# Kernel tuning notes

Measured on AMD Instinct MI355X. Metric: run time of the kernel, lower is better.

Reference implementation:

```python
import jax, jax.numpy as jnp
import numpy as np

N_PAPER = 100000
N_AUTHOR = 50000
E = 800000
D_IN, D_HID, D_OUT = 128, 128, 64


def seg_max(x, src, dst, num_segments):
    # adj_t.matmul(x, reduce='max'): per-destination max over neighbor features;
    # destinations with no in-edges get 0 (torch_sparse convention).
    m = jax.ops.segment_max(x[src], dst, num_segments=num_segments)
    return jnp.where(jnp.isneginf(m), jnp.zeros((), m.dtype), m)


def setup_inputs() -> dict:
    key = jax.random.key(0)
    ks = jax.random.split(key, 32)
    inp = {}
    inp['x_paper'] = jax.random.normal(ks[0], (N_PAPER, D_IN), jnp.float32)
    inp['emb_author'] = jax.random.normal(ks[1], (N_AUTHOR, D_IN), jnp.float32)
    inp['writes_src'] = jax.random.randint(ks[2], (E,), 0, N_AUTHOR, jnp.int32)
    inp['writes_dst'] = jax.random.randint(ks[3], (E,), 0, N_PAPER, jnp.int32)
    inp['cites_src'] = jax.random.randint(ks[4], (E,), 0, N_PAPER, jnp.int32)
    inp['cites_dst'] = jax.random.randint(ks[5], (E,), 0, N_PAPER, jnp.int32)
    inp['wb_src'] = jax.random.randint(ks[6], (E,), 0, N_PAPER, jnp.int32)
    inp['wb_dst'] = jax.random.randint(ks[7], (E,), 0, N_AUTHOR, jnp.int32)

    def lin_w(k, din, dout):
        s = 1.0 / np.sqrt(din)
        return jax.random.uniform(k, (din, dout), jnp.float32, -s, s)

    # layer 1: D_IN -> D_HID
    inp['w1_rel_writes'] = lin_w(ks[8], D_IN, D_HID)
    inp['w1_rel_cites'] = lin_w(ks[9], D_IN, D_HID)
    inp['w1_rel_wb'] = lin_w(ks[10], D_IN, D_HID)
    inp['w1_root_paper'] = lin_w(ks[11], D_IN, D_HID)
    inp['b1_root_paper'] = jnp.zeros((D_HID,), jnp.float32)
    inp['w1_root_author'] = lin_w(ks[12], D_IN, D_HID)
    inp['b1_root_author'] = jnp.zeros((D_HID,), jnp.float32)
    # layer 2: D_HID -> D_OUT
    inp['w2_rel_writes'] = lin_w(ks[13], D_HID, D_OUT)
    inp['w2_rel_cites'] = lin_w(ks[14], D_HID, D_OUT)
    inp['w2_rel_wb'] = lin_w(ks[15], D_HID, D_OUT)
    inp['w2_root_paper'] = lin_w(ks[16], D_HID, D_OUT)
    inp['b2_root_paper'] = jnp.zeros((D_OUT,), jnp.float32)
    inp['w2_root_author'] = lin_w(ks[17], D_HID, D_OUT)
    inp['b2_root_author'] = jnp.zeros((D_OUT,), jnp.float32)
    return inp


def _conv(xp, xa, edges, w_writes, w_cites, w_wb, w_rp, b_rp, w_ra, b_ra):
    writes_src, writes_dst, cites_src, cites_dst, wb_src, wb_dst = edges
    out_p = xp @ w_rp + b_rp
    out_a = xa @ w_ra + b_ra
    out_p = out_p + seg_max(xa, writes_src, writes_dst, N_PAPER) @ w_writes
    out_p = out_p + seg_max(xp, cites_src, cites_dst, N_PAPER) @ w_cites
    out_a = out_a + seg_max(xp, wb_src, wb_dst, N_AUTHOR) @ w_wb
    return out_p, out_a


def reference(x_paper, emb_author,
              writes_src, writes_dst, cites_src, cites_dst, wb_src, wb_dst,
              w1_rel_writes, w1_rel_cites, w1_rel_wb,
              w1_root_paper, b1_root_paper, w1_root_author, b1_root_author,
              w2_rel_writes, w2_rel_cites, w2_rel_wb,
              w2_root_paper, b2_root_paper, w2_root_author, b2_root_author):
    edges = (writes_src, writes_dst, cites_src, cites_dst, wb_src, wb_dst)
    hp, ha = _conv(x_paper, emb_author, edges,
                   w1_rel_writes, w1_rel_cites, w1_rel_wb,
                   w1_root_paper, b1_root_paper, w1_root_author, b1_root_author)
    hp, ha = jax.nn.relu(hp), jax.nn.relu(ha)  # dropout p=0 -> identity
    return _conv(hp, ha, edges,
                 w2_rel_writes, w2_rel_cites, w2_rel_wb,
                 w2_root_paper, b2_root_paper, w2_root_author, b2_root_author)
```

## Files before the change

### kernel.cpp

```cpp
#include <hip/hip_runtime.h>


#define DI 128
#define NP 100000
#define NA 50000
#define EPB 4096
#define MAXBIN 391

typedef short s8v __attribute__((ext_vector_type(8)));
typedef float f32x4 __attribute__((ext_vector_type(4)));

__device__ __forceinline__ unsigned short bf16_rne(float f) {
  unsigned int fb = __float_as_uint(f);
  fb += 0x7FFFu + ((fb >> 16) & 1u);
  return (unsigned short)(fb >> 16);
}

__global__ __launch_bounds__(256) void cvt2_k(const float* __restrict__ Xp,
                                              unsigned short* __restrict__ Yp, int n4p,
                                              const float* __restrict__ Xa,
                                              unsigned short* __restrict__ Ya, int n4a) {
  int i = blockIdx.x * 256 + threadIdx.x;
  const float* X; unsigned short* Y;
  if (i < n4p) { X = Xp; Y = Yp; }
  else { i -= n4p; if (i >= n4a) return; X = Xa; Y = Ya; }
  float4 f = reinterpret_cast<const float4*>(X)[i];
  ushort4 o;
  o.x = bf16_rne(f.x); o.y = bf16_rne(f.y); o.z = bf16_rne(f.z); o.w = bf16_rne(f.w);
  reinterpret_cast<ushort4*>(Y)[i] = o;
}

struct R3Args {
  const int* src[3]; const int* dst[3];
  int* bh[3]; int* bhs[3];
  unsigned int* tmp[3];
  int* bkt[3]; int* cnt[3]; int* rs[3];
  int E[3]; int N[3]; int nbin[3]; int NB[3];
};

__global__ __launch_bounds__(256) void radix_s1_k(R3Args a) {
  int y = blockIdx.y, blk = blockIdx.x;
  int NB = a.NB[y];
  if (blk >= NB) return;
  __shared__ int hist[MAXBIN];
  int nbin = a.nbin[y];
  for (int i = threadIdx.x; i < nbin; i += 256) hist[i] = 0;
  __syncthreads();
  int e0 = blk * EPB, e1 = min(e0 + EPB, a.E[y]);
  const int* dst = a.dst[y];
  for (int e = e0 + threadIdx.x; e < e1; e += 256)
    atomicAdd(&hist[dst[e] >> 8], 1);
  __syncthreads();
  int* bh = a.bh[y];
  for (int i = threadIdx.x; i < nbin; i += 256) bh[i * NB + blk] = hist[i];
}

__global__ __launch_bounds__(256) void radix_x1_k(R3Args a) {
  int y = blockIdx.y, blk = blockIdx.x;
  int NB = a.NB[y];
  if (blk >= NB) return;
  __shared__ int cur[MAXBIN];
  int nbin = a.nbin[y];
  const int* bhs = a.bhs[y];
  for (int i = threadIdx.x; i < nbin; i += 256) cur[i] = bhs[i * NB + blk];
  __syncthreads();
  int e0 = blk * EPB, e1 = min(e0 + EPB, a.E[y]);
  const int* dst = a.dst[y];
  const int* src = a.src[y];
  unsigned int* tmp = a.tmp[y];
  for (int e = e0 + threadIdx.x; e < e1; e += 256) {
    int d = dst[e];
    int pos = atomicAdd(&cur[d >> 8], 1);
    tmp[pos] = ((unsigned int)(d & 255) << 24) | (unsigned int)src[e];
  }
}

__global__ __launch_bounds__(256) void radix_p2_k(R3Args a) {
  int y = blockIdx.y, bin = blockIdx.x;
  if (bin >= a.nbin[y]) return;
  __shared__ int hist[256], scn[256], cursor[256];
  int t = threadIdx.x;
  hist[t] = 0;
  __syncthreads();
  const int* bhs = a.bhs[y];
  int NB = a.NB[y];
  int base = bhs[bin * NB];
  int end  = (bin + 1 < a.nbin[y]) ? bhs[(bin + 1) * NB] : a.E[y];
  const unsigned int* tmp = a.tmp[y];
  for (int i = base + t; i < end; i += 256)
    atomicAdd(&hist[tmp[i] >> 24], 1);
  __syncthreads();
  int v = hist[t];
  scn[t] = v; __syncthreads();
  int acc = v;
  for (int o = 1; o < 256; o <<= 1) {
    int u = (t >= o) ? scn[t - o] : 0;
    __syncthreads();
    acc += u; scn[t] = acc;
    __syncthreads();
  }
  int ex = acc - v;
  cursor[t] = ex;
  int d = bin * 256 + t;
  if (d < a.N[y]) { a.cnt[y][d] = v; a.rs[y][d] = base + ex; }
  __syncthreads();
  int* bkt = a.bkt[y];
  for (int i = base + t; i < end; i += 256) {
    unsigned int p = tmp[i];
    int pos = atomicAdd(&cursor[p >> 24], 1);
    bkt[base + pos] = (int)(p & 0xFFFFFFu);
  }
}

struct S3Args {
  const int* cnt[3]; int* bsum[3]; int* rs[3];
  int n[3]; int nb[3];
};

__global__ __launch_bounds__(256) void blocksum3_k(S3Args a) {
  int y = blockIdx.y;
  int n = a.n[y];
  if (blockIdx.x * 1024 >= n) return;
  __shared__ int red[256];
  int t = threadIdx.x;
  int base = blockIdx.x * 1024 + t * 4;
  int s = 0;
  #pragma unroll
  for (int i = 0; i < 4; ++i) { int idx = base + i; if (idx < n) s += a.cnt[y][idx]; }
  red[t] = s; __syncthreads();
  #pragma unroll
  for (int o = 128; o > 0; o >>= 1) { if (t < o) red[t] += red[t + o]; __syncthreads(); }
  if (t == 0) a.bsum[y][blockIdx.x] = red[0];
}

__global__ __launch_bounds__(256) void partials3_k(S3Args a) {
  __shared__ int sm[256];
  int y = blockIdx.x;
  int nb = a.nb[y];
  int t = threadIdx.x;
  int v = (t < nb) ? a.bsum[y][t] : 0;
  sm[t] = v; __syncthreads();
  int acc = v;
  for (int o = 1; o < 256; o <<= 1) {
    int u = (t >= o) ? sm[t - o] : 0;
    __syncthreads();
    acc += u; sm[t] = acc;
    __syncthreads();
  }
  if (t < nb) a.bsum[y][t] = acc - v;
}

__global__ __launch_bounds__(256) void scanwrite3_k(S3Args a) {
  int y = blockIdx.y;
  int n = a.n[y];
  if (blockIdx.x * 1024 >= n) return;
  __shared__ int ts[256];
  int t = threadIdx.x;
  int base = blockIdx.x * 1024 + t * 4;
  int v[4]; int s = 0;
  #pragma unroll
  for (int i = 0; i < 4; ++i) { int idx = base + i; v[i] = (idx < n) ? a.cnt[y][idx] : 0; s += v[i]; }
  ts[t] = s; __syncthreads();
  int inc = s;
  for (int o = 1; o < 256; o <<= 1) {
    int u = (t >= o) ? ts[t - o] : 0;
    __syncthreads();
    inc += u; ts[t] = inc;
    __syncthreads();
  }
  int p = a.bsum[y][blockIdx.x] + inc - s;
  #pragma unroll
  for (int i = 0; i < 4; ++i) { int idx = base + i; if (idx < n) { a.rs[y][idx] = p; p += v[i]; } }
}

struct G3Args {
  const int* cnt[3]; const int* rs[3]; const int* bkt[3];
  const unsigned short* X[3]; unsigned short* S[3];
  int N[3];
};

__global__ __launch_bounds__(256) void gather3_k(G3Args a) {
  const int y = blockIdx.y;
  const int lane = threadIdx.x & 63;
  const int wave = threadIdx.x >> 6;
  const int g = lane >> 4, lg = lane & 15;
  const int d = blockIdx.x * 16 + wave * 4 + g;
  if (d >= a.N[y]) return;

  unsigned short* So = a.S[y] + (size_t)d * DI + lg * 8;
  const int deg = a.cnt[y][d];
  if (deg == 0) {
    uint4 z; z.x = z.y = z.z = z.w = 0u;
    *reinterpret_cast<uint4*>(So) = z;
    return;
  }
  const int* bp = a.bkt[y] + a.rs[y][d];
  const unsigned short* X = a.X[y];

  float ml[4], mh[4];
  #pragma unroll
  for (int j = 0; j < 4; ++j) { ml[j] = -3.4e38f; mh[j] = -3.4e38f; }

  int s0 = bp[0];
  for (int e = 0; e < deg; e += 4) {
    int s1 = (e + 1 < deg) ? bp[e + 1] : s0;
    int s2 = (e + 2 < deg) ? bp[e + 2] : s0;
    int s3 = (e + 3 < deg) ? bp[e + 3] : s0;
    int sn = (e + 4 < deg) ? bp[e + 4] : s0;
    uint4 r0 = *reinterpret_cast<const uint4*>(X + (size_t)s0 * DI + lg * 8);
    uint4 r1 = *reinterpret_cast<const uint4*>(X + (size_t)s1 * DI + lg * 8);
    uint4 r2 = *reinterpret_cast<const uint4*>(X + (size_t)s2 * DI + lg * 8);
    uint4 r3 = *reinterpret_cast<const uint4*>(X + (size_t)s3 * DI + lg * 8);
    unsigned int w0[4] = {r0.x, r0.y, r0.z, r0.w};
    unsigned int w1[4] = {r1.x, r1.y, r1.z, r1.w};
    unsigned int w2[4] = {r2.x, r2.y, r2.z, r2.w};
    unsigned int w3[4] = {r3.x, r3.y, r3.z, r3.w};
    #pragma unroll
    for (int j = 0; j < 4; ++j) {
      float a0 = fmaxf(__uint_as_float(w0[j] << 16), __uint_as_float(w1[j] << 16));
      float a1 = fmaxf(__uint_as_float(w2[j] << 16), __uint_as_float(w3[j] << 16));
      ml[j] = fmaxf(ml[j], fmaxf(a0, a1));
      float b0 = fmaxf(__uint_as_float(w0[j] & 0xFFFF0000u), __uint_as_float(w1[j] & 0xFFFF0000u));
      float b1 = fmaxf(__uint_as_float(w2[j] & 0xFFFF0000u), __uint_as_float(w3[j] & 0xFFFF0000u));
      mh[j] = fmaxf(mh[j], fmaxf(b0, b1));
    }
    s0 = sn;
  }
  uint4 o;
  o.x = (__float_as_uint(ml[0]) >> 16) | (__float_as_uint(mh[0]) & 0xFFFF0000u);
  o.y = (__float_as_uint(ml[1]) >> 16) | (__float_as_uint(mh[1]) & 0xFFFF0000u);
  o.z = (__float_as_uint(ml[2]) >> 16) | (__float_as_uint(mh[2]) & 0xFFFF0000u);
  o.w = (__float_as_uint(ml[3]) >> 16) | (__float_as_uint(mh[3]) & 0xFFFF0000u);
  *reinterpret_cast<uint4*>(So) = o;
}

struct WArgs {
  const float* w[10];
  unsigned short* wf[10];
};
__global__ __launch_bounds__(256) void warrange_k(WArgs args) {
  int widx = blockIdx.y;
  int OUTi = (widx < 5) ? 128 : 64;
  int CF = OUTi / 16;
  int nt = 4 * CF * 64;
  int t = blockIdx.x * 256 + threadIdx.x;
  if (t >= nt) return;
  int lane = t & 63, tmp = t >> 6;
  int cf = tmp % CF, kc = tmp / CF;
  int k0 = kc * 32 + (lane >> 4) * 8;
  int c  = cf * 16 + (lane & 15);
  const float* w = args.w[widx];
  s8v v;
  #pragma unroll
  for (int i = 0; i < 8; ++i) v[i] = (short)bf16_rne(w[(k0 + i) * OUTi + c]);
  *(reinterpret_cast<s8v*>(args.wf[widx]) + t) = v;
}

template<int CF>
__device__ __forceinline__ void mfma_accum(const unsigned short* __restrict__ A,
                                           const unsigned short* __restrict__ W,
                                           f32x4* acc, size_t arow, int lane, int half) {
  const s8v* a = reinterpret_cast<const s8v*>(A + arow * DI + half * 8);
  const s8v* w = reinterpret_cast<const s8v*>(W) + lane;
  #pragma unroll
  for (int kc = 0; kc < 4; ++kc) {
    s8v av = a[kc * 4];
    #pragma unroll
    for (int cf = 0; cf < CF; ++cf)
      acc[cf] = __builtin_amdgcn_mfma_f32_16x16x32_bf16(av, w[(kc * CF + cf) * 64], acc[cf], 0, 0, 0);
  }
}

struct GemmPairArgs {
  const unsigned short *A0[2], *W0[2], *A1[2], *W1[2], *A2, *W2;
  const float* bias[2];
  void* out[2];
  int N[2];
  int blocks0;
};

template<int OUT, bool RELU, bool OUT_BF16>
__global__ __launch_bounds__(256) void gemm_pair_k(GemmPairArgs g) {
  constexpr int CF = OUT / 16;
  const int p = (blockIdx.x >= (unsigned)g.blocks0) ? 1 : 0;
  const int brow = blockIdx.x - (p ? g.blocks0 : 0);
  const int N = g.N[p];
  const int lane = threadIdx.x & 63;
  const int wave = threadIdx.x >> 6;
  const int row0 = brow * 64 + wave * 16;
  if (row0 >= N) return;
  const int rl = lane & 15, half = lane >> 4;
  const size_t arow = (size_t)(row0 + rl);

  f32x4 acc[CF];
  #pragma unroll
  for (int i = 0; i < CF; ++i) acc[i] = f32x4{0.f, 0.f, 0.f, 0.f};

  mfma_accum<CF>(g.A0[p], g.W0[p], acc, arow, lane, half);
  mfma_accum<CF>(g.A1[p], g.W1[p], acc, arow, lane, half);
  if (!p) mfma_accum<CF>(g.A2, g.W2, acc, arow, lane, half);

  const float* bias = g.bias[p];
  #pragma unroll
  for (int cf = 0; cf < CF; ++cf) {
    float bv = bias[cf * 16 + rl];
    #pragma unroll
    for (int j = 0; j < 4; ++j) {
      int r = row0 + half * 4 + j;
      if (r >= N) continue;
      float v = acc[cf][j] + bv;
      if (RELU) v = v > 0.f ? v : 0.f;
      size_t idx = (size_t)r * OUT + cf * 16 + rl;
      if (OUT_BF16) ((unsigned short*)g.out[p])[idx] = bf16_rne(v);
      else          ((float*)g.out[p])[idx] = v;
    }
  }
}

extern "C" void kernel_launch(void* const* d_in, const int* in_sizes, int n_in,
                              void* d_out, int out_size, void* d_ws, size_t ws_size,
                              hipStream_t stream) {
  const float* xp = (const float*)d_in[0];
  const float* xa = (const float*)d_in[1];
  const int* wsrc = (const int*)d_in[2];
  const int* wdst = (const int*)d_in[3];
  const int* csrc = (const int*)d_in[4];
  const int* cdst = (const int*)d_in[5];
  const int* bsrc = (const int*)d_in[6];
  const int* bdst = (const int*)d_in[7];
  const int Ew = in_sizes[2], Ec = in_sizes[4], Eb = in_sizes[6];

  const float* w1w  = (const float*)d_in[8];
  const float* w1c  = (const float*)d_in[9];
  const float* w1wb = (const float*)d_in[10];
  const float* w1rp = (const float*)d_in[11];
  const float* b1rp = (const float*)d_in[12];
  const float* w1ra = (const float*)d_in[13];
  const float* b1ra = (const float*)d_in[14];
  const float* w2w  = (const float*)d_in[15];
  const float* w2c  = (const float*)d_in[16];
  const float* w2wb = (const float*)d_in[17];
  const float* w2rp = (const float*)d_in[18];
  const float* b2rp = (const float*)d_in[19];
  const float* w2ra = (const float*)d_in[20];
  const float* b2ra = (const float*)d_in[21];

  char* ws = (char*)d_ws;
  unsigned short* xpb = (unsigned short*)(ws + 0);
  unsigned short* xab = (unsigned short*)(ws + 25600000);
  unsigned short* hp  = (unsigned short*)(ws + 38400000);
  unsigned short* ha  = (unsigned short*)(ws + 64000000);
  unsigned short* S_w = (unsigned short*)(ws + 76800000);
  unsigned short* S_c = (unsigned short*)(ws + 102400000);
  unsigned short* S_b = (unsigned short*)(ws + 128000000);
  int* bkt_w = (int*)(ws + 140800000);
  int* bkt_c = (int*)(ws + 144000000);
  int* bkt_b = (int*)(ws + 147200000);
  int* cnt_w = (int*)(ws + 150400000);
  int* cnt_c = (int*)(ws + 150800000);
  int* cnt_b = (int*)(ws + 151200000);
  int* rs_w  = (int*)(ws + 151400000);
  int* rs_c  = (int*)(ws + 151800000);
  int* rs_b  = (int*)(ws + 152200000);
  int* bsum_w = (int*)(ws + 152400000);
  int* bsum_c = (int*)(ws + 152404096);
  int* bsum_b = (int*)(ws + 152408192);
  unsigned short* wf = (unsigned short*)(ws + 152412288);
  unsigned int* tmp_w = (unsigned int*)(ws + 152660000);
  unsigned int* tmp_c = (unsigned int*)(ws + 155860000);
  unsigned int* tmp_b = (unsigned int*)(ws + 159060000);
  int* bh_w  = (int*)(ws + 76800000);
  int* bh_c  = (int*)(ws + 77110000);
  int* bh_b  = (int*)(ws + 77420000);
  int* bhs_w = (int*)(ws + 77580000);
  int* bhs_c = (int*)(ws + 77890000);
  int* bhs_b = (int*)(ws + 78200000);

  unsigned short* WF[10];
  size_t off = 0;
  for (int i = 0; i < 10; ++i) {
    WF[i] = wf + off;
    off += (i < 5) ? (size_t)128 * 128 : (size_t)128 * 64;
  }
  WArgs wa;
  const float* wsrcs[10] = {w1w, w1c, w1wb, w1rp, w1ra, w2w, w2c, w2wb, w2rp, w2ra};
  for (int i = 0; i < 10; ++i) { wa.w[i] = wsrcs[i]; wa.wf[i] = WF[i]; }

  float* outP = (float*)d_out;
  float* outA = outP + (size_t)NP * 64;

  const int gP = (NP + 63) / 64, gA = (NA + 63) / 64;
  const int gG = (NP + 15) / 16;

  R3Args ra;
  ra.src[0] = wsrc; ra.dst[0] = wdst; ra.E[0] = Ew; ra.N[0] = NP;
  ra.src[1] = csrc; ra.dst[1] = cdst; ra.E[1] = Ec; ra.N[1] = NP;
  ra.src[2] = bsrc; ra.dst[2] = bdst; ra.E[2] = Eb; ra.N[2] = NA;
  ra.bh[0] = bh_w; ra.bh[1] = bh_c; ra.bh[2] = bh_b;
  ra.bhs[0] = bhs_w; ra.bhs[1] = bhs_c; ra.bhs[2] = bhs_b;
  ra.tmp[0] = tmp_w; ra.tmp[1] = tmp_c; ra.tmp[2] = tmp_b;
  ra.bkt[0] = bkt_w; ra.bkt[1] = bkt_c; ra.bkt[2] = bkt_b;
  ra.cnt[0] = cnt_w; ra.cnt[1] = cnt_c; ra.cnt[2] = cnt_b;
  ra.rs[0] = rs_w; ra.rs[1] = rs_c; ra.rs[2] = rs_b;
  int gSX = 0, gSC = 0, maxbin = 0;
  for (int y = 0; y < 3; ++y) {
    ra.nbin[y] = (ra.N[y] + 255) >> 8;
    ra.NB[y] = (ra.E[y] + EPB - 1) / EPB;
    if (ra.NB[y] > gSX) gSX = ra.NB[y];
    if (ra.nbin[y] > maxbin) maxbin = ra.nbin[y];
  }
  S3Args sa;
  sa.bsum[0] = bsum_w; sa.bsum[1] = bsum_c; sa.bsum[2] = bsum_b;
  for (int y = 0; y < 3; ++y) {
    sa.cnt[y] = ra.bh[y]; sa.rs[y] = ra.bhs[y];
    sa.n[y] = ra.nbin[y] * ra.NB[y];
    sa.nb[y] = (sa.n[y] + 1023) / 1024;
    if (sa.nb[y] > gSC) gSC = sa.nb[y];
  }

  G3Args g1, g2;
  for (int i = 0; i < 3; ++i) {
    g1.cnt[i] = g2.cnt[i] = (i == 0) ? cnt_w : (i == 1) ? cnt_c : cnt_b;
    g1.rs[i]  = g2.rs[i]  = (i == 0) ? rs_w  : (i == 1) ? rs_c  : rs_b;
    g1.bkt[i] = g2.bkt[i] = (i == 0) ? bkt_w : (i == 1) ? bkt_c : bkt_b;
    g1.S[i]   = g2.S[i]   = (i == 0) ? S_w   : (i == 1) ? S_c   : S_b;
    g1.N[i]   = g2.N[i]   = (i == 2) ? NA : NP;
  }
  g1.X[0] = xab; g1.X[1] = xpb; g1.X[2] = xpb;
  g2.X[0] = ha;  g2.X[1] = hp;  g2.X[2] = hp;

  GemmPairArgs p1, p2;
  p1.A0[0] = xpb; p1.W0[0] = WF[3]; p1.A1[0] = S_w; p1.W1[0] = WF[0]; p1.A2 = S_c; p1.W2 = WF[1];
  p1.bias[0] = b1rp; p1.out[0] = hp; p1.N[0] = NP;
  p1.A0[1] = xab; p1.W0[1] = WF[4]; p1.A1[1] = S_b; p1.W1[1] = WF[2];
  p1.bias[1] = b1ra; p1.out[1] = ha; p1.N[1] = NA;
  p1.blocks0 = gP;
  p2.A0[0] = hp; p2.W0[0] = WF[8]; p2.A1[0] = S_w; p2.W1[0] = WF[5]; p2.A2 = S_c; p2.W2 = WF[6];
  p2.bias[0] = b2rp; p2.out[0] = outP; p2.N[0] = NP;
  p2.A0[1] = ha; p2.W0[1] = WF[9]; p2.A1[1] = S_b; p2.W1[1] = WF[7];
  p2.bias[1] = b2ra; p2.out[1] = outA; p2.N[1] = NA;
  p2.blocks0 = gP;

  const int n4p = NP * DI / 4, n4a = NA * DI / 4;

  warrange_k<<<dim3(8, 10), 256, 0, stream>>>(wa);
  cvt2_k<<<(n4p + n4a + 255) / 256, 256, 0, stream>>>(xp, xpb, n4p, xa, xab, n4a);

  radix_s1_k<<<dim3(gSX, 3), 256, 0, stream>>>(ra);
  blocksum3_k<<<dim3(gSC, 3), 256, 0, stream>>>(sa);
  partials3_k<<<3, 256, 0, stream>>>(sa);
  scanwrite3_k<<<dim3(gSC, 3), 256, 0, stream>>>(sa);
  radix_x1_k<<<dim3(gSX, 3), 256, 0, stream>>>(ra);
  radix_p2_k<<<dim3(maxbin, 3), 256, 0, stream>>>(ra);

  gather3_k<<<dim3(gG, 3), 256, 0, stream>>>(g1);
  gemm_pair_k<128, true, true><<<gP + gA, 256, 0, stream>>>(p1);

  gather3_k<<<dim3(gG, 3), 256, 0, stream>>>(g2);
  gemm_pair_k<64, false, false><<<gP + gA, 256, 0, stream>>>(p2);
}
```

Before: 356.2 us.

## Fuse bucket placement, weight rearrange and bf16 conversion into one launch

```diff
diff --git a/kernel.cpp b/kernel.cpp
--- a/kernel.cpp
+++ b/kernel.cpp
@@ -14,20 +14,6 @@
   unsigned int fb = __float_as_uint(f);
   fb += 0x7FFFu + ((fb >> 16) & 1u);
   return (unsigned short)(fb >> 16);
-}
-
-__global__ __launch_bounds__(256) void cvt2_k(const float* __restrict__ Xp,
-                                              unsigned short* __restrict__ Yp, int n4p,
-                                              const float* __restrict__ Xa,
-                                              unsigned short* __restrict__ Ya, int n4a) {
-  int i = blockIdx.x * 256 + threadIdx.x;
-  const float* X; unsigned short* Y;
-  if (i < n4p) { X = Xp; Y = Yp; }
-  else { i -= n4p; if (i >= n4a) return; X = Xa; Y = Ya; }
-  float4 f = reinterpret_cast<const float4*>(X)[i];
-  ushort4 o;
-  o.x = bf16_rne(f.x); o.y = bf16_rne(f.y); o.z = bf16_rne(f.z); o.w = bf16_rne(f.w);
-  reinterpret_cast<ushort4*>(Y)[i] = o;
 }
 
 struct R3Args {
@@ -75,41 +61,87 @@
   }
 }
 
-__global__ __launch_bounds__(256) void radix_p2_k(R3Args a) {
-  int y = blockIdx.y, bin = blockIdx.x;
-  if (bin >= a.nbin[y]) return;
-  __shared__ int hist[256], scn[256], cursor[256];
+struct WArgs {
+  const float* w[10];
+  unsigned short* wf[10];
+};
+
+struct P2CArgs {
+  R3Args ra;
+  WArgs wa;
+  const float* Xp; unsigned short* Yp; int n4p;
+  const float* Xa; unsigned short* Ya; int n4a;
+  int p2Blocks;
+  int maxbin;
+};
+
+__global__ __launch_bounds__(256) void p2cvt_k(P2CArgs a) {
+  int bid = blockIdx.x;
   int t = threadIdx.x;
-  hist[t] = 0;
-  __syncthreads();
-  const int* bhs = a.bhs[y];
-  int NB = a.NB[y];
-  int base = bhs[bin * NB];
-  int end  = (bin + 1 < a.nbin[y]) ? bhs[(bin + 1) * NB] : a.E[y];
-  const unsigned int* tmp = a.tmp[y];
-  for (int i = base + t; i < end; i += 256)
-    atomicAdd(&hist[tmp[i] >> 24], 1);
-  __syncthreads();
-  int v = hist[t];
-  scn[t] = v; __syncthreads();
-  int acc = v;
-  for (int o = 1; o < 256; o <<= 1) {
-    int u = (t >= o) ? scn[t - o] : 0;
-    __syncthreads();
-    acc += u; scn[t] = acc;
-    __syncthreads();
-  }
-  int ex = acc - v;
-  cursor[t] = ex;
-  int d = bin * 256 + t;
-  if (d < a.N[y]) { a.cnt[y][d] = v; a.rs[y][d] = base + ex; }
-  __syncthreads();
-  int* bkt = a.bkt[y];
-  for (int i = base + t; i < end; i += 256) {
-    unsigned int p = tmp[i];
-    int pos = atomicAdd(&cursor[p >> 24], 1);
-    bkt[base + pos] = (int)(p & 0xFFFFFFu);
-  }
+  if (bid < a.p2Blocks) {
+    int y = bid / a.maxbin, bin = bid % a.maxbin;
+    if (bin >= a.ra.nbin[y]) return;
+    __shared__ int hist[256], scn[256], cursor[256];
+    hist[t] = 0;
+    __syncthreads();
+    const int* bhs = a.ra.bhs[y];
+    int NB = a.ra.NB[y];
+    int base = bhs[bin * NB];
+    int end  = (bin + 1 < a.ra.nbin[y]) ? bhs[(bin + 1) * NB] : a.ra.E[y];
+    const unsigned int* tmp = a.ra.tmp[y];
+    for (int i = base + t; i < end; i += 256)
+      atomicAdd(&hist[tmp[i] >> 24], 1);
+    __syncthreads();
+    int v = hist[t];
+    scn[t] = v; __syncthreads();
+    int acc = v;
+    for (int o = 1; o < 256; o <<= 1) {
+      int u = (t >= o) ? scn[t - o] : 0;
+      __syncthreads();
+      acc += u; scn[t] = acc;
+      __syncthreads();
+    }
+    int ex = acc - v;
+    cursor[t] = ex;
+    int d = bin * 256 + t;
+    if (d < a.ra.N[y]) { a.ra.cnt[y][d] = v; a.ra.rs[y][d] = base + ex; }
+    __syncthreads();
+    int* bkt = a.ra.bkt[y];
+    for (int i = base + t; i < end; i += 256) {
+      unsigned int p = tmp[i];
+      int pos = atomicAdd(&cursor[p >> 24], 1);
+      bkt[base + pos] = (int)((p & 0xFFFFFFu) << 8);
+    }
+    return;
+  }
+  bid -= a.p2Blocks;
+  if (bid < 80) {
+    int widx = bid >> 3;
+    int OUTi = (widx < 5) ? 128 : 64;
+    int CF = OUTi / 16;
+    int nt = 4 * CF * 64;
+    int tg = (bid & 7) * 256 + t;
+    if (tg >= nt) return;
+    int lane = tg & 63, tmp2 = tg >> 6;
+    int cf = tmp2 % CF, kc = tmp2 / CF;
+    int k0 = kc * 32 + (lane >> 4) * 8;
+    int c  = cf * 16 + (lane & 15);
+    const float* w = a.wa.w[widx];
+    s8v v;
+    #pragma unroll
+    for (int i = 0; i < 8; ++i) v[i] = (short)bf16_rne(w[(k0 + i) * OUTi + c]);
+    *(reinterpret_cast<s8v*>(a.wa.wf[widx]) + tg) = v;
+    return;
+  }
+  bid -= 80;
+  int i = bid * 256 + t;
+  const float* X; unsigned short* Y;
+  if (i < a.n4p) { X = a.Xp; Y = a.Yp; }
+  else { i -= a.n4p; if (i >= a.n4a) return; X = a.Xa; Y = a.Ya; }
+  float4 f = reinterpret_cast<const float4*>(X)[i];
+  ushort4 o;
+  o.x = bf16_rne(f.x); o.y = bf16_rne(f.y); o.z = bf16_rne(f.z); o.w = bf16_rne(f.w);
+  reinterpret_cast<ushort4*>(Y)[i] = o;
 }
 
 struct S3Args {
@@ -195,7 +227,7 @@
     return;
   }
   const int* bp = a.bkt[y] + a.rs[y][d];
-  const unsigned short* X = a.X[y];
+  const char* Xb = reinterpret_cast<const char*>(a.X[y]) + lg * 16;
 
   float ml[4], mh[4];
   #pragma unroll
@@ -207,22 +239,22 @@
     int s2 = (e + 2 < deg) ? bp[e + 2] : s0;
     int s3 = (e + 3 < deg) ? bp[e + 3] : s0;
     int sn = (e + 4 < deg) ? bp[e + 4] : s0;
-    uint4 r0 = *reinterpret_cast<const uint4*>(X + (size_t)s0 * DI + lg * 8);
-    uint4 r1 = *reinterpret_cast<const uint4*>(X + (size_t)s1 * DI + lg * 8);
-    uint4 r2 = *reinterpret_cast<const uint4*>(X + (size_t)s2 * DI + lg * 8);
-    uint4 r3 = *reinterpret_cast<const uint4*>(X + (size_t)s3 * DI + lg * 8);
+    uint4 r0 = *reinterpret_cast<const uint4*>(Xb + s0);
+    uint4 r1 = *reinterpret_cast<const uint4*>(Xb + s1);
+    uint4 r2 = *reinterpret_cast<const uint4*>(Xb + s2);
+    uint4 r3 = *reinterpret_cast<const uint4*>(Xb + s3);
     unsigned int w0[4] = {r0.x, r0.y, r0.z, r0.w};
     unsigned int w1[4] = {r1.x, r1.y, r1.z, r1.w};
     unsigned int w2[4] = {r2.x, r2.y, r2.z, r2.w};
     unsigned int w3[4] = {r3.x, r3.y, r3.z, r3.w};
     #pragma unroll
     for (int j = 0; j < 4; ++j) {
-      float a0 = fmaxf(__uint_as_float(w0[j] << 16), __uint_as_float(w1[j] << 16));
-      float a1 = fmaxf(__uint_as_float(w2[j] << 16), __uint_as_float(w3[j] << 16));
-      ml[j] = fmaxf(ml[j], fmaxf(a0, a1));
-      float b0 = fmaxf(__uint_as_float(w0[j] & 0xFFFF0000u), __uint_as_float(w1[j] & 0xFFFF0000u));
-      float b1 = fmaxf(__uint_as_float(w2[j] & 0xFFFF0000u), __uint_as_float(w3[j] & 0xFFFF0000u));
-      mh[j] = fmaxf(mh[j], fmaxf(b0, b1));
+      float tl = fmaxf(fmaxf(__uint_as_float(w0[j] << 16), __uint_as_float(w1[j] << 16)),
+                       __uint_as_float(w2[j] << 16));
+      ml[j] = fmaxf(fmaxf(ml[j], __uint_as_float(w3[j] << 16)), tl);
+      float th = fmaxf(fmaxf(__uint_as_float(w0[j] & 0xFFFF0000u), __uint_as_float(w1[j] & 0xFFFF0000u)),
+                       __uint_as_float(w2[j] & 0xFFFF0000u));
+      mh[j] = fmaxf(fmaxf(mh[j], __uint_as_float(w3[j] & 0xFFFF0000u)), th);
     }
     s0 = sn;
   }
@@ -232,28 +264,6 @@
   o.z = (__float_as_uint(ml[2]) >> 16) | (__float_as_uint(mh[2]) & 0xFFFF0000u);
   o.w = (__float_as_uint(ml[3]) >> 16) | (__float_as_uint(mh[3]) & 0xFFFF0000u);
   *reinterpret_cast<uint4*>(So) = o;
-}
-
-struct WArgs {
-  const float* w[10];
-  unsigned short* wf[10];
-};
-__global__ __launch_bounds__(256) void warrange_k(WArgs args) {
-  int widx = blockIdx.y;
-  int OUTi = (widx < 5) ? 128 : 64;
-  int CF = OUTi / 16;
-  int nt = 4 * CF * 64;
-  int t = blockIdx.x * 256 + threadIdx.x;
-  if (t >= nt) return;
-  int lane = t & 63, tmp = t >> 6;
-  int cf = tmp % CF, kc = tmp / CF;
-  int k0 = kc * 32 + (lane >> 4) * 8;
-  int c  = cf * 16 + (lane & 15);
-  const float* w = args.w[widx];
-  s8v v;
-  #pragma unroll
-  for (int i = 0; i < 8; ++i) v[i] = (short)bf16_rne(w[(k0 + i) * OUTi + c]);
-  *(reinterpret_cast<s8v*>(args.wf[widx]) + t) = v;
 }
 
 template<int CF>
@@ -382,9 +392,6 @@
     WF[i] = wf + off;
     off += (i < 5) ? (size_t)128 * 128 : (size_t)128 * 64;
   }
-  WArgs wa;
-  const float* wsrcs[10] = {w1w, w1c, w1wb, w1rp, w1ra, w2w, w2c, w2wb, w2rp, w2ra};
-  for (int i = 0; i < 10; ++i) { wa.w[i] = wsrcs[i]; wa.wf[i] = WF[i]; }
 
   float* outP = (float*)d_out;
   float* outA = outP + (size_t)NP * 64;
@@ -418,6 +425,17 @@
     if (sa.nb[y] > gSC) gSC = sa.nb[y];
   }
 
+  const int n4p = NP * DI / 4, n4a = NA * DI / 4;
+  P2CArgs pc;
+  pc.ra = ra;
+  const float* wsrcs[10] = {w1w, w1c, w1wb, w1rp, w1ra, w2w, w2c, w2wb, w2rp, w2ra};
+  for (int i = 0; i < 10; ++i) { pc.wa.w[i] = wsrcs[i]; pc.wa.wf[i] = WF[i]; }
+  pc.Xp = xp; pc.Yp = xpb; pc.n4p = n4p;
+  pc.Xa = xa; pc.Ya = xab; pc.n4a = n4a;
+  pc.maxbin = maxbin;
+  pc.p2Blocks = 3 * maxbin;
+  const int gPC = pc.p2Blocks + 80 + (n4p + n4a + 255) / 256;
+
   G3Args g1, g2;
   for (int i = 0; i < 3; ++i) {
     g1.cnt[i] = g2.cnt[i] = (i == 0) ? cnt_w : (i == 1) ? cnt_c : cnt_b;
@@ -441,17 +459,12 @@
   p2.bias[1] = b2ra; p2.out[1] = outA; p2.N[1] = NA;
   p2.blocks0 = gP;
 
-  const int n4p = NP * DI / 4, n4a = NA * DI / 4;
-
-  warrange_k<<<dim3(8, 10), 256, 0, stream>>>(wa);
-  cvt2_k<<<(n4p + n4a + 255) / 256, 256, 0, stream>>>(xp, xpb, n4p, xa, xab, n4a);
-
   radix_s1_k<<<dim3(gSX, 3), 256, 0, stream>>>(ra);
   blocksum3_k<<<dim3(gSC, 3), 256, 0, stream>>>(sa);
   partials3_k<<<3, 256, 0, stream>>>(sa);
   scanwrite3_k<<<dim3(gSC, 3), 256, 0, stream>>>(sa);
   radix_x1_k<<<dim3(gSX, 3), 256, 0, stream>>>(ra);
-  radix_p2_k<<<dim3(maxbin, 3), 256, 0, stream>>>(ra);
+  p2cvt_k<<<gPC, 256, 0, stream>>>(pc);
 
   gather3_k<<<dim3(gG, 3), 256, 0, stream>>>(g1);
   gemm_pair_k<128, true, true><<<gP + gA, 256, 0, stream>>>(p1);
```

New measurement: 344.6 us. 3.3% less time.
